# Optimization experiments

Measured on AMD Instinct MI355X. Metric: run time of the kernel, lower is better.

The kernel has to match this reference:

```python
import jax, jax.numpy as jnp
import numpy as np

EPS = 1e-6
FRAME_SEQLEN = 1560          # hardcoded in source kv-cache path
LOCAL_ATTN_SIZE = 4
MAX_ATTN = LOCAL_ATTN_SIZE * FRAME_SEQLEN  # 6240
NUM_HEADS = 12


def _ln(x, w=None, b=None):
    mu = jnp.mean(x, axis=-1, keepdims=True)
    var = jnp.mean(jnp.square(x - mu), axis=-1, keepdims=True)
    y = (x - mu) * jax.lax.rsqrt(var + EPS)
    return y * w + b if w is not None else y


def _rms(x, w):
    return x * jax.lax.rsqrt(jnp.mean(jnp.square(x), axis=-1, keepdims=True) + EPS) * w


def _rope_tables(freqs_real, freqs_imag, nf, hh, ww, start_frame, c):
    # split freqs columns into temporal / height / width parts, as in causal_rope_apply
    s0 = c - 2 * (c // 3)
    s1 = c // 3
    def build(tab):
        f0 = tab[start_frame:start_frame + nf, :s0]       # [nf, s0]
        f1 = tab[:hh, s0:s0 + s1]                          # [hh, s1]
        f2 = tab[:ww, s0 + s1:]                            # [ww, s1]
        return jnp.concatenate([
            jnp.broadcast_to(f0[:, None, None, :], (nf, hh, ww, s0)),
            jnp.broadcast_to(f1[None, :, None, :], (nf, hh, ww, s1)),
            jnp.broadcast_to(f2[None, None, :, :], (nf, hh, ww, s1)),
        ], axis=-1).reshape(nf * hh * ww, 1, c)
    return build(freqs_real), build(freqs_imag)


def _causal_rope(x, cos, sin):
    # x: [B, L, n, d] with interleaved (real, imag) pairs; cos/sin: [1, L, 1, c]
    B, L, n, d = x.shape
    c = d // 2
    xr = x.reshape(B, L, n, c, 2)
    a, b = xr[..., 0], xr[..., 1]
    out = jnp.stack([a * cos - b * sin, a * sin + b * cos], axis=-1)
    return out.reshape(B, L, n, d)


def _sdpa(q, k, v):
    scale = q.shape[-1] ** -0.5
    s = jnp.einsum('bqhd,bkhd->bhqk', q, k) * scale
    a = jax.nn.softmax(s, axis=-1)
    return jnp.einsum('bhqk,bkhd->bqhd', a, v)


def _forward(hidden_states, encoder_hidden_states, temb, freqs_real, freqs_imag,
             k_cache, v_cache, scale_shift_table,
             Wq, bq, Wk, bk, Wv, bv, Wo, bo, norm_q_w, norm_k_w,
             saln_w, saln_b,
             cWq, cbq, cWk, cbk, cWv, cbv, cWo, cbo, c_norm_q_w, c_norm_k_w,
             W1, b1, W2, b2,
             current_start, grid_h, grid_w):
    B, L, D = hidden_states.shape
    nf = temb.shape[1]
    fs = L // nf                     # == FRAME_SEQLEN
    H = NUM_HEADS
    hd = D // H
    c = hd // 2
    x = hidden_states.astype(jnp.float32)

    # AdaLN modulation per frame
    e = scale_shift_table + temb                     # [B, nf, 6, D]
    shift, scale, gate = e[:, :, 0:1], e[:, :, 1:2], e[:, :, 2:3]
    c_shift, c_scale, c_gate = e[:, :, 3:4], e[:, :, 4:5], e[:, :, 5:6]

    nh = (_ln(x).reshape(B, nf, fs, D) * (1 + scale) + shift).reshape(B, L, D)

    # self-attn projections + rms_norm_across_heads qk norm
    q = _rms(nh @ Wq.T + bq, norm_q_w).reshape(B, L, H, hd)
    k = _rms(nh @ Wk.T + bk, norm_k_w).reshape(B, L, H, hd)
    v = (nh @ Wv.T + bv).reshape(B, L, H, hd)

    # causal RoPE with temporal offset current_start // 1560
    start_frame = current_start // FRAME_SEQLEN
    cos, sin = _rope_tables(freqs_real, freqs_imag, nf, grid_h, grid_w, start_frame, c)
    cos, sin = cos[None], sin[None]                  # [1, L, 1, c]
    rq = _causal_rope(q, cos, sin)
    rk = _causal_rope(k, cos, sin)

    # kv-cache update (no-eviction branch: num_new + local_end_prev == cache size)
    kc = jax.lax.stop_gradient(k_cache).at[:, current_start:current_start + L].set(rk)
    vc = jax.lax.stop_gradient(v_cache).at[:, current_start:current_start + L].set(v)
    local_end = current_start + L
    win_lo = max(0, local_end - MAX_ATTN)
    attn = _sdpa(rq, kc[:, win_lo:local_end], vc[:, win_lo:local_end]).reshape(B, L, D)
    attn = attn @ Wo.T + bo

    # gated residual + affine LN (self_attn_residual_norm)
    x = x + (attn.reshape(B, nf, fs, D) * gate).reshape(B, L, D)
    n2 = _ln(x, saln_w, saln_b)

    # T2V cross attention
    ctx = encoder_hidden_states.astype(jnp.float32)
    Lc = ctx.shape[1]
    cq = _rms(n2 @ cWq.T + cbq, c_norm_q_w).reshape(B, L, H, hd)
    ck = _rms(ctx @ cWk.T + cbk, c_norm_k_w).reshape(B, Lc, H, hd)
    cv = (ctx @ cWv.T + cbv).reshape(B, Lc, H, hd)
    ca = _sdpa(cq, ck, cv).reshape(B, L, D) @ cWo.T + cbo

    # residual + LN with c_scale/c_shift modulation (cross_attn_residual_norm)
    x = x + ca
    n3 = (_ln(x).reshape(B, nf, fs, D) * (1 + c_scale) + c_shift).reshape(B, L, D)

    # FFN (gelu tanh) + gated residual (MulAdd)
    ff = jax.nn.gelu(n3 @ W1.T + b1, approximate=True) @ W2.T + b2
    x = x + (ff.reshape(B, nf, fs, D) * c_gate).reshape(B, L, D)
    return x


def setup_inputs() -> dict:
    key = jax.random.key(0)
    D, FF, H = 1536, 8960, NUM_HEADS
    NF, FS = 2, FRAME_SEQLEN
    L = NF * FS
    CACHE = MAX_ATTN
    CTX = 512
    hd = D // H
    c = hd // 2
    ks = iter(jax.random.split(key, 40))
    def nrm(shape, s=1.0):
        return jax.random.normal(next(ks), shape, jnp.float32) * s

    def part(dim):
        inv = 1.0 / (10000.0 ** (np.arange(0, dim, 2, dtype=np.float64) / dim))
        f = np.outer(np.arange(1024, dtype=np.float64), inv)
        return np.cos(f), np.sin(f)
    c0, s0 = part(2 * (c - 2 * (c // 3)))
    c1, s1 = part(2 * (c // 3))
    c2, s2 = part(2 * (c // 3))
    freqs_real = jnp.asarray(np.concatenate([c0, c1, c2], axis=1), jnp.float32)  # [1024, 64]
    freqs_imag = jnp.asarray(np.concatenate([s0, s1, s2], axis=1), jnp.float32)

    return dict(
        hidden_states=nrm((1, L, D)),
        encoder_hidden_states=nrm((1, CTX, D)),
        temb=nrm((1, NF, 6, D), 0.5),
        freqs_real=freqs_real, freqs_imag=freqs_imag,
        k_cache=nrm((1, CACHE, H, hd), 0.5),
        v_cache=nrm((1, CACHE, H, hd), 0.5),
        scale_shift_table=nrm((1, 6, D), D ** -0.5),
        Wq=nrm((D, D), 0.02), bq=jnp.zeros((D,), jnp.float32),
        Wk=nrm((D, D), 0.02), bk=jnp.zeros((D,), jnp.float32),
        Wv=nrm((D, D), 0.02), bv=jnp.zeros((D,), jnp.float32),
        Wo=nrm((D, D), 0.02), bo=jnp.zeros((D,), jnp.float32),
        norm_q_w=jnp.ones((D,), jnp.float32), norm_k_w=jnp.ones((D,), jnp.float32),
        saln_w=jnp.ones((D,), jnp.float32), saln_b=jnp.zeros((D,), jnp.float32),
        cWq=nrm((D, D), 0.02), cbq=jnp.zeros((D,), jnp.float32),
        cWk=nrm((D, D), 0.02), cbk=jnp.zeros((D,), jnp.float32),
        cWv=nrm((D, D), 0.02), cbv=jnp.zeros((D,), jnp.float32),
        cWo=nrm((D, D), 0.02), cbo=jnp.zeros((D,), jnp.float32),
        c_norm_q_w=jnp.ones((D,), jnp.float32), c_norm_k_w=jnp.ones((D,), jnp.float32),
        W1=nrm((FF, D), 0.02), b1=jnp.zeros((FF,), jnp.float32),
        W2=nrm((D, FF), 0.02), b2=jnp.zeros((D,), jnp.float32),
        current_start=2 * FS, grid_h=30, grid_w=52,
    )


def reference(hidden_states, encoder_hidden_states, temb, freqs_real, freqs_imag,
              k_cache, v_cache, scale_shift_table,
              Wq, bq, Wk, bk, Wv, bv, Wo, bo, norm_q_w, norm_k_w,
              saln_w, saln_b,
              cWq, cbq, cWk, cbk, cWv, cbv, cWo, cbo, c_norm_q_w, c_norm_k_w,
              W1, b1, W2, b2,
              current_start, grid_h, grid_w):
    return _forward(hidden_states, encoder_hidden_states, temb, freqs_real, freqs_imag,
                    k_cache, v_cache, scale_shift_table,
                    Wq, bq, Wk, bk, Wv, bv, Wo, bo, norm_q_w, norm_k_w,
                    saln_w, saln_b,
                    cWq, cbq, cWk, cbk, cWv, cbv, cWo, cbo, c_norm_q_w, c_norm_k_w,
                    W1, b1, W2, b2,
                    current_start, grid_h, grid_w)
```

## Files before the change

kernel.cpp:

```cpp
#include <hip/hip_runtime.h>
#include <hip/hip_bf16.h>
#include <stdint.h>

typedef uint16_t u16;
typedef uint32_t u32;
typedef float    f32x4  __attribute__((ext_vector_type(4)));
typedef __bf16   bf16x8 __attribute__((ext_vector_type(8)));
typedef u16      u16x8  __attribute__((ext_vector_type(8)));
typedef u16      u16x4  __attribute__((ext_vector_type(4)));
typedef float    f32x4v __attribute__((ext_vector_type(4)));

#define KSTR 6272
#define KHS  802816

__device__ __forceinline__ u16 f2bf(float f) {
    u32 u = __builtin_bit_cast(u32, f);
    u32 r = u + 0x7fffu + ((u >> 16) & 1u);
    return (u16)(r >> 16);
}
__device__ __forceinline__ float bfbits2f(u32 ubits) {
    return __builtin_bit_cast(float, ubits << 16);
}
__device__ __forceinline__ u32 cvtpk(float a, float b) {
    u32 r;
    asm("v_cvt_pk_bf16_f32 %0, %1, %2" : "=v"(r) : "v"(a), "v"(b));
    return r;
}
__device__ __forceinline__ bf16x8 loadb8(const u16* p) {
    u16x8 u = *(const u16x8*)p;
    return __builtin_bit_cast(bf16x8, u);
}
__device__ __forceinline__ f32x4 mfma16(bf16x8 a, bf16x8 b, f32x4 c) {
    return __builtin_amdgcn_mfma_f32_16x16x32_bf16(a, b, c, 0, 0, 0);
}
__device__ __forceinline__ void gload16(const u16* gp, u16* lp) {
    __builtin_amdgcn_global_load_lds((const __attribute__((address_space(1))) void*)gp,
                                     (__attribute__((address_space(3))) void*)lp, 16, 0, 0);
}
__device__ __forceinline__ float blockSum(float v, volatile float* buf, int t) {
#pragma unroll
    for (int o = 1; o < 64; o <<= 1) v += __shfl_xor(v, o);
    if ((t & 63) == 0) buf[t >> 6] = v;
    __syncthreads();
    float r = buf[0] + buf[1] + buf[2] + buf[3];
    __syncthreads();
    return r;
}

struct ConvJob { const float* s; u16* d; int n4; };
struct ConvJobs { ConvJob j[12]; int cnt; };

__global__ void k_conv(ConvJobs js) {
    int tid = blockIdx.x * blockDim.x + threadIdx.x;
    int stride = gridDim.x * blockDim.x;
    for (int q = 0; q < js.cnt; q++) {
        const f32x4v* s = (const f32x4v*)js.j[q].s;
        u16x4* d = (u16x4*)js.j[q].d;
        int n4 = js.j[q].n4;
        for (int i = tid; i < n4; i += stride) {
            f32x4v v = s[i];
            u16x4 o;
            o[0] = f2bf(v[0]); o[1] = f2bf(v[1]); o[2] = f2bf(v[2]); o[3] = f2bf(v[3]);
            d[i] = o;
        }
    }
}

__global__ void k_mod(const float* __restrict__ sst, const float* __restrict__ temb, float* __restrict__ e) {
    int i = blockIdx.x * 256 + threadIdx.x;
    if (i < 18432) e[i] = sst[i % 9216] + temb[i];
}

__global__ void k_cachecvt(const float* __restrict__ kc, const float* __restrict__ vc,
                           u16* __restrict__ Ka, u16* __restrict__ Va) {
    int b = blockIdx.x;
    int hd = (b % 6) * 256 + threadIdx.x;
    int p0 = (b / 6) * 4;
    int h = hd >> 7, d = hd & 127;
    u16x4 vv;
#pragma unroll
    for (int j = 0; j < 4; j++) {
        long src = (long)(p0 + j) * 1536 + hd;
        Ka[(long)h * KHS + (long)(p0 + j) * 128 + d] = f2bf(kc[src]);
        vv[j] = f2bf(vc[src]);
    }
    *(u16x4*)&Va[(long)h * KHS + (long)d * KSTR + p0] = vv;
}

__global__ void k_zpad(u16* __restrict__ Ka, u16* __restrict__ Va) {
    int i = blockIdx.x * 256 + threadIdx.x;
    int h = i >> 12, rem = i & 4095, row = rem >> 7, d = rem & 127;
    Ka[(long)h * KHS + (long)(6240 + row) * 128 + d] = 0;
    Va[(long)h * KHS + (long)d * KSTR + 6240 + row] = 0;
}

__global__ __launch_bounds__(256) void k_ln(const float* __restrict__ x, u16* __restrict__ out,
                                            const float* __restrict__ mulp, const float* __restrict__ addp,
                                            int perFrame, int plusOne) {
    __shared__ float buf[4];
    const int row = blockIdx.x, t = threadIdx.x;
    const float* xr = x + (long)row * 1536;
    float v[6];
    float s = 0.f;
#pragma unroll
    for (int k = 0; k < 6; k++) { v[k] = xr[t + k * 256]; s += v[k]; }
    s = blockSum(s, buf, t);
    float mu = s * (1.f / 1536.f);
    float q = 0.f;
#pragma unroll
    for (int k = 0; k < 6; k++) { float d = v[k] - mu; q += d * d; }
    q = blockSum(q, buf, t);
    float inv = rsqrtf(q * (1.f / 1536.f) + 1e-6f);
    const int fo = perFrame ? (row / 1560) * 9216 : 0;
    u16* orow = out + (long)row * 1536;
    float add1 = plusOne ? 1.f : 0.f;
#pragma unroll
    for (int k = 0; k < 6; k++) {
        int c = t + k * 256;
        float m = mulp[fo + c] + add1;
        float y = (v[k] - mu) * inv * m + addp[fo + c];
        orow[c] = f2bf(y);
    }
}

__global__ __launch_bounds__(256) void k_rmsrope(const u16* __restrict__ in, int ld, int colOff,
                                                 const float* __restrict__ bias,
                                                 const float* __restrict__ w,
                                                 u16* __restrict__ out, long headStride,
                                                 const float* __restrict__ fr, const float* __restrict__ fi,
                                                 int doRope) {
    __shared__ float buf[4];
    const int row = blockIdx.x, t = threadIdx.x;
    const u32* xr = (const u32*)(in + (long)row * ld + colOff);
    const float2* b2 = (const float2*)bias;
    float px[3], py[3];
    float ss = 0.f;
#pragma unroll
    for (int i = 0; i < 3; i++) {
        u32 u = xr[t * 3 + i];
        float2 bb = b2[t * 3 + i];
        px[i] = bfbits2f(u & 0xffffu) + bb.x;
        py[i] = bfbits2f(u >> 16) + bb.y;
        ss += px[i] * px[i] + py[i] * py[i];
    }
    ss = blockSum(ss, buf, t);
    float inv = rsqrtf(ss * (1.f / 1536.f) + 1e-6f);
    int frame = 0, gh = 0, gw = 0;
    if (doRope) { frame = row / 1560; int rem = row - frame * 1560; gh = rem / 52; gw = rem - gh * 52; }
    const float2* w2 = (const float2*)w;
#pragma unroll
    for (int i = 0; i < 3; i++) {
        int jg = t * 3 + i;
        int hh = jg >> 6, j = jg & 63;
        float2 ww = w2[jg];
        float a = px[i] * inv * ww.x, b = py[i] * inv * ww.y;
        float oa = a, ob = b;
        if (doRope) {
            int fidx = (j < 22) ? (2 + frame) : ((j < 43) ? gh : gw);
            float cs = fr[fidx * 64 + j], sn = fi[fidx * 64 + j];
            oa = a * cs - b * sn;
            ob = a * sn + b * cs;
        }
        u16* dst = out + (long)hh * headStride + (long)row * 128 + j * 2;
        dst[0] = f2bf(oa);
        dst[1] = f2bf(ob);
    }
}

__global__ void k_scatterT(const u16* __restrict__ in, int ld, int colOff,
                           const float* __restrict__ bias, u16* __restrict__ outT,
                           int vstride, int posOff) {
    int hd = blockIdx.x * 256 + threadIdx.x;
    int r0 = blockIdx.y * 4;
    int h = hd >> 7, d = hd & 127;
    float bi = bias[hd];
    u16x4 pk;
#pragma unroll
    for (int j = 0; j < 4; j++)
        pk[j] = f2bf(bfbits2f(in[(long)(r0 + j) * ld + colOff + hd]) + bi);
    *(u16x4*)&outT[(long)h * 128 * vstride + (long)d * vstride + posOff + r0] = pk;
}

struct GemmP {
    const u16* A; const u16* B; void* C;
    const float* bias; const float* gate; const float* resid;
    int M, N, K, ldA, ldB, ldC, kChunk;
};

template <int EPI, int BM>
__global__ __launch_bounds__(256) void k_gemm(GemmP g) {
    constexpr int WM = BM / 2;
    constexpr int TM = BM / 32;
    __shared__ alignas(16) u16 As[BM * 32];
    __shared__ alignas(16) u16 Bs[128 * 32];
    const int t = threadIdx.x;
    const int w = t >> 6, l = t & 63, lr = l & 15, lg = l >> 4;
    const int wm = w >> 1, wn = w & 1;
    const long m0 = (long)blockIdx.y * BM, n0 = (long)blockIdx.x * 128;
    f32x4 acc[TM][4];
#pragma unroll
    for (int a = 0; a < TM; a++)
#pragma unroll
        for (int b = 0; b < 4; b++) acc[a][b] = f32x4{0.f, 0.f, 0.f, 0.f};

    const int rowU = t >> 2, c8 = t & 3;
    long arow[2], brow[2];
#pragma unroll
    for (int i = 0; i < 2; i++) {
        long r = m0 + rowU + i * 64;
        if (r > (long)g.M - 1) r = g.M - 1;
        arow[i] = r;
        brow[i] = n0 + rowU + i * 64;
    }

    const int kBeg = blockIdx.z * g.kChunk;
    const int kEnd = min(g.K, kBeg + g.kChunk);
    for (int k0 = kBeg; k0 < kEnd; k0 += 32) {
        __syncthreads();
#pragma unroll
        for (int i = 0; i < BM / 64; i++)
            gload16(g.A + arow[i] * (long)g.ldA + k0 + c8 * 8, &As[(i * 256 + w * 64) * 8]);
#pragma unroll
        for (int i = 0; i < 2; i++)
            gload16(g.B + brow[i] * (long)g.ldB + k0 + c8 * 8, &Bs[(i * 256 + w * 64) * 8]);
        __syncthreads();
        bf16x8 am[TM], bn[4];
#pragma unroll
        for (int mi = 0; mi < TM; mi++) am[mi] = loadb8(&As[(wm * WM + mi * 16 + lr) * 32 + lg * 8]);
#pragma unroll
        for (int ni = 0; ni < 4; ni++) bn[ni] = loadb8(&Bs[(wn * 64 + ni * 16 + lr) * 32 + lg * 8]);
#pragma unroll
        for (int mi = 0; mi < TM; mi++)
#pragma unroll
            for (int ni = 0; ni < 4; ni++)
                acc[mi][ni] = mfma16(am[mi], bn[ni], acc[mi][ni]);
    }

#pragma unroll
    for (int mi = 0; mi < TM; mi++) {
#pragma unroll
        for (int ni = 0; ni < 4; ni++) {
            long col = n0 + wn * 64 + ni * 16 + lr;
            float bi = g.bias ? g.bias[col] : 0.f;
#pragma unroll
            for (int r = 0; r < 4; r++) {
                long row = m0 + wm * WM + mi * 16 + lg * 4 + r;
                if (row >= g.M) continue;
                float v = acc[mi][ni][r] + bi;
                if constexpr (EPI == 0) {
                    ((float*)g.C)[row * g.ldC + col] = v;
                } else if constexpr (EPI == 1) {
                    ((u16*)g.C)[row * g.ldC + col] = f2bf(v);
                } else if constexpr (EPI == 2) {
                    float x3 = v * v * v;
                    float gl = 0.5f * v * (1.f + tanhf(0.79788456080286536f * (v + 0.044715f * x3)));
                    ((u16*)g.C)[row * g.ldC + col] = f2bf(gl);
                } else if constexpr (EPI == 3) {
                    float gt = g.gate ? g.gate[(row / 1560) * 9216 + col] : 1.f;
                    ((float*)g.C)[row * g.ldC + col] = g.resid[row * g.ldC + col] + v * gt;
                } else {
                    ((float*)g.C)[(long)blockIdx.z * ((long)g.M * g.ldC) + row * g.ldC + col] = v;
                }
            }
        }
    }
}

__global__ void k_gcomb(const float* __restrict__ P, int S, long MN4,
                        const float* __restrict__ bias, const float* __restrict__ gate,
                        const float* __restrict__ resid, float* __restrict__ out) {
    long i = (long)blockIdx.x * 256 + threadIdx.x;
    if (i >= MN4) return;
    f32x4v a = ((const f32x4v*)P)[i];
#pragma unroll 3
    for (int s = 1; s < S; s++) {
        f32x4v b = ((const f32x4v*)P)[(long)s * MN4 + i];
        a[0] += b[0]; a[1] += b[1]; a[2] += b[2]; a[3] += b[3];
    }
    long e0 = i * 4;
    int col = (int)(e0 % 1536);
    int fo = (int)((e0 / 1536) / 1560) * 9216;
    f32x4v r = ((const f32x4v*)resid)[i];
#pragma unroll
    for (int j = 0; j < 4; j++)
        r[j] += (a[j] + bias[col + j]) * gate[fo + col + j];
    ((f32x4v*)out)[i] = r;
}

__global__ void k_sumbf(const float* __restrict__ P, int S, long N4, u16* __restrict__ out) {
    long i = (long)blockIdx.x * 256 + threadIdx.x;
    if (i >= N4) return;
    f32x4v a = ((const f32x4v*)P)[i];
#pragma unroll 3
    for (int s = 1; s < S; s++) {
        f32x4v b = ((const f32x4v*)P)[(long)s * N4 + i];
        a[0] += b[0]; a[1] += b[1]; a[2] += b[2]; a[3] += b[3];
    }
    u16x4 o;
    o[0] = f2bf(a[0]); o[1] = f2bf(a[1]); o[2] = f2bf(a[2]); o[3] = f2bf(a[3]);
    ((u16x4*)out)[i] = o;
}

__global__ __launch_bounds__(256) void k_flash(const u16* __restrict__ Qb, const u16* __restrict__ Kb,
                                               const u16* __restrict__ Vtg,
                                               u16* __restrict__ Opart, float2* __restrict__ ms,
                                               int kvStride, int kvLen, int qlen,
                                               int splitIters, int totIters) {
    __shared__ alignas(16) u16 Kt[64 * 136];
    __shared__ alignas(16) u16 Vt[128 * 72];
    __shared__ alignas(16) u16 Pt[4][32 * 40];
    const int t = threadIdx.x;
    const int w = t >> 6, l = t & 63, lr = l & 15, lg = l >> 4;
    const int head = blockIdx.y, z = blockIdx.z;
    const long q0 = (long)blockIdx.x * 128;
    const u16* Qh = Qb + (long)head * qlen * 128;
    const u16* Kh = Kb + (long)head * (long)kvStride * 128;
    const u16* Vh = Vtg + (long)head * (long)kvStride * 128;
    constexpr float SCL2 = 0.08838834764831845f * 1.44269504088896f;

    bf16x8 aq[2][4];
#pragma unroll
    for (int wq = 0; wq < 2; wq++)
#pragma unroll
        for (int c = 0; c < 4; c++) {
            long row = q0 + w * 32 + wq * 16 + lr;
            if (row > (long)qlen - 1) row = qlen - 1;
            aq[wq][c] = loadb8(Qh + row * 128 + c * 32 + lg * 8);
        }

    f32x4 o[2][8];
    float mrow[2] = {-1e30f, -1e30f}, srow[2] = {0.f, 0.f};
#pragma unroll
    for (int wq = 0; wq < 2; wq++)
#pragma unroll
        for (int db = 0; db < 8; db++) o[wq][db] = f32x4{0.f, 0.f, 0.f, 0.f};

    const int krow = t >> 2, kcol = (t & 3) * 32;
    const int vrow = t >> 1, vcol = (t & 1) * 32;
    u16x8 pkr[4], pvr[4];

    const int it0 = z * splitIters;
    const int itN = min(totIters, it0 + splitIters);

    auto loadTile = [&](int kt) {
        long k0 = (long)kt * 64;
        const u16* kp = Kh + (k0 + krow) * 128 + kcol;
#pragma unroll
        for (int j = 0; j < 4; j++) pkr[j] = *(const u16x8*)(kp + j * 8);
        const u16* vp = Vh + (long)vrow * kvStride + k0 + vcol;
#pragma unroll
        for (int j = 0; j < 4; j++) pvr[j] = *(const u16x8*)(vp + j * 8);
    };
    auto writeTile = [&]() {
#pragma unroll
        for (int j = 0; j < 4; j++) *(u16x8*)&Kt[krow * 136 + kcol + j * 8] = pkr[j];
#pragma unroll
        for (int j = 0; j < 4; j++) *(u16x8*)&Vt[vrow * 72 + vcol + j * 8] = pvr[j];
    };

    loadTile(it0);
    writeTile();
    __syncthreads();

    for (int kt = it0; kt < itN; kt++) {
        const bool hasNext = (kt + 1 < itN);
        if (hasNext) loadTile(kt + 1);
        const int lim = kvLen - kt * 64;

#pragma unroll
        for (int h2 = 0; h2 < 2; h2++) {
            f32x4 s[2][2];
            __builtin_amdgcn_s_setprio(1);
#pragma unroll
            for (int kh = 0; kh < 2; kh++) {
                bf16x8 kf[4];
#pragma unroll
                for (int cb = 0; cb < 4; cb++)
                    kf[cb] = loadb8(&Kt[(h2 * 32 + kh * 16 + lr) * 136 + cb * 32 + lg * 8]);
#pragma unroll
                for (int wq = 0; wq < 2; wq++) {
                    f32x4 acc = f32x4{0.f, 0.f, 0.f, 0.f};
#pragma unroll
                    for (int cb = 0; cb < 4; cb++) acc = mfma16(kf[cb], aq[wq][cb], acc);
                    s[wq][kh] = acc;
                }
            }
            __builtin_amdgcn_s_setprio(0);

            const int sublim = lim - h2 * 32;
#pragma unroll
            for (int wq = 0; wq < 2; wq++) {
                float pm = fmaxf(fmaxf(fmaxf(s[wq][0][0], s[wq][0][1]), fmaxf(s[wq][0][2], s[wq][0][3])),
                                 fmaxf(fmaxf(s[wq][1][0], s[wq][1][1]), fmaxf(s[wq][1][2], s[wq][1][3])));
                pm = fmaxf(pm, __shfl_xor(pm, 16));
                pm = fmaxf(pm, __shfl_xor(pm, 32));
                float pm2 = pm * SCL2;
                if (__any(pm2 > mrow[wq] + 8.f)) {
                    float nm = fmaxf(mrow[wq], pm2);
                    float fsc = exp2f(mrow[wq] - nm);
                    mrow[wq] = nm;
                    srow[wq] *= fsc;
#pragma unroll
                    for (int db = 0; db < 8; db++) {
                        f32x4 t4 = o[wq][db];
                        t4[0] *= fsc; t4[1] *= fsc; t4[2] *= fsc; t4[3] *= fsc;
                        o[wq][db] = t4;
                    }
                }
                float p[8];
#pragma unroll
                for (int kh = 0; kh < 2; kh++)
#pragma unroll
                    for (int r = 0; r < 4; r++)
                        p[kh * 4 + r] = exp2f(fmaf(s[wq][kh][r], SCL2, -mrow[wq]));
                if (sublim < 32) {
#pragma unroll
                    for (int kh = 0; kh < 2; kh++)
#pragma unroll
                        for (int r = 0; r < 4; r++)
                            if (kh * 16 + lg * 4 + r >= sublim) p[kh * 4 + r] = 0.f;
                }
                float ts = ((p[0] + p[1]) + (p[2] + p[3])) + ((p[4] + p[5]) + (p[6] + p[7]));
                ts += __shfl_xor(ts, 16);
                ts += __shfl_xor(ts, 32);
                srow[wq] += ts;
                u32 w0 = cvtpk(p[0], p[1]), w1 = cvtpk(p[2], p[3]);
                u32 w2 = cvtpk(p[4], p[5]), w3 = cvtpk(p[6], p[7]);
                u16* pp = &Pt[w][(wq * 16 + lr) * 40 + lg * 4];
                *(u32*)pp = w0;
                *(u32*)(pp + 2) = w1;
                *(u32*)(pp + 16) = w2;
                *(u32*)(pp + 18) = w3;
            }

            bf16x8 pb0 = loadb8(&Pt[w][lr * 40 + lg * 8]);
            bf16x8 pb1 = loadb8(&Pt[w][(16 + lr) * 40 + lg * 8]);
            __builtin_amdgcn_s_setprio(1);
#pragma unroll
            for (int db = 0; db < 8; db++) {
                bf16x8 vf = loadb8(&Vt[(db * 16 + lr) * 72 + h2 * 32 + lg * 8]);
                o[0][db] = mfma16(vf, pb0, o[0][db]);
                o[1][db] = mfma16(vf, pb1, o[1][db]);
            }
            __builtin_amdgcn_s_setprio(0);
        }
        __syncthreads();
        if (hasNext) writeTile();
        __syncthreads();
    }

    const long part = ((long)z * 12 + head) * qlen;
#pragma unroll
    for (int wq = 0; wq < 2; wq++) {
        long row = q0 + w * 32 + wq * 16 + lr;
        if (row < qlen) {
            if (lg == 0) {
                float2 v; v.x = mrow[wq]; v.y = srow[wq];
                ms[part + row] = v;
            }
#pragma unroll
            for (int db = 0; db < 8; db++) {
                u16x4 pk;
#pragma unroll
                for (int r = 0; r < 4; r++) pk[r] = f2bf(o[wq][db][r]);
                *(u16x4*)&Opart[(part + row) * 128 + db * 16 + lg * 4] = pk;
            }
        }
    }
}

__global__ __launch_bounds__(256) void k_combine(const u16* __restrict__ Opart, const float2* __restrict__ ms,
                                                 u16* __restrict__ Ob, int qlen, int S) {
    int idx = blockIdx.x * 4 + (threadIdx.x >> 6);
    int l = threadIdx.x & 63;
    int h = idx / qlen, q = idx - h * qlen;
    float2 mm[6];
    float M = -1e30f;
    for (int s = 0; s < S; s++) {
        mm[s] = ms[((long)s * 12 + h) * qlen + q];
        M = fmaxf(M, mm[s].x);
    }
    float den = 0.f, a0 = 0.f, a1 = 0.f;
    for (int s = 0; s < S; s++) {
        float wgt = exp2f(mm[s].x - M);
        den += wgt * mm[s].y;
        u32 two = *(const u32*)&Opart[(((long)s * 12 + h) * qlen + q) * 128 + l * 2];
        a0 += wgt * bfbits2f(two & 0xffffu);
        a1 += wgt * bfbits2f(two >> 16);
    }
    float inv = 1.f / den;
    u32 o = ((u32)f2bf(a1 * inv) << 16) | (u32)f2bf(a0 * inv);
    *(u32*)&Ob[(long)q * 1536 + h * 128 + l * 2] = o;
}

extern "C" void kernel_launch(void* const* d_in, const int* in_sizes, int n_in,
                              void* d_out, int out_size, void* d_ws, size_t ws_size,
                              hipStream_t stream) {
    const float* hs    = (const float*)d_in[0];
    const float* ctx   = (const float*)d_in[1];
    const float* temb  = (const float*)d_in[2];
    const float* fr    = (const float*)d_in[3];
    const float* fi    = (const float*)d_in[4];
    const float* kcache= (const float*)d_in[5];
    const float* vcache= (const float*)d_in[6];
    const float* sst   = (const float*)d_in[7];
    const float* Wq = (const float*)d_in[8],  *bq = (const float*)d_in[9];
    const float* Wk = (const float*)d_in[10], *bk = (const float*)d_in[11];
    const float* Wv = (const float*)d_in[12], *bv = (const float*)d_in[13];
    const float* Wo = (const float*)d_in[14], *bo = (const float*)d_in[15];
    const float* nqw = (const float*)d_in[16], *nkw = (const float*)d_in[17];
    const float* salnw = (const float*)d_in[18], *salnb = (const float*)d_in[19];
    const float* cWq = (const float*)d_in[20], *cbq = (const float*)d_in[21];
    const float* cWk = (const float*)d_in[22], *cbk = (const float*)d_in[23];
    const float* cWv = (const float*)d_in[24], *cbv = (const float*)d_in[25];
    const float* cWo = (const float*)d_in[26], *cbo = (const float*)d_in[27];
    const float* cnqw = (const float*)d_in[28], *cnkw = (const float*)d_in[29];
    const float* W1 = (const float*)d_in[30], *b1 = (const float*)d_in[31];
    const float* W2 = (const float*)d_in[32], *b2 = (const float*)d_in[33];
    float* out = (float*)d_out;

    char* base = (char*)d_ws;
    size_t off = 0;
    auto alloc = [&](size_t bytes) -> char* {
        char* p = base + off;
        off = (off + bytes + 255) & ~(size_t)255;
        return p;
    };
    float* e   = (float*)alloc(18432 * 4);
    u16* nbuf  = (u16*)alloc((size_t)3120 * 1536 * 2);
    u16* lin   = (u16*)alloc((size_t)3120 * 4608 * 2);
    u16* Qb    = (u16*)alloc((size_t)12 * 3120 * 128 * 2);
    u16* Ka    = (u16*)alloc((size_t)12 * KSTR * 128 * 2);
    u16* Va    = (u16*)alloc((size_t)12 * KSTR * 128 * 2);
    u16* attnb = (u16*)alloc((size_t)3120 * 1536 * 2);
    float* X1  = (float*)alloc((size_t)3120 * 1536 * 4);
    u16* CKb   = (u16*)alloc((size_t)12 * 512 * 128 * 2);
    u16* CVt   = (u16*)alloc((size_t)12 * 512 * 128 * 2);
    u16* H1    = (u16*)alloc((size_t)3120 * 8960 * 2);
    u16* wqkv_b= (u16*)alloc((size_t)4608 * 1536 * 2);
    u16* wo_b  = (u16*)alloc((size_t)1536 * 1536 * 2);
    u16* cwq_b = (u16*)alloc((size_t)1536 * 1536 * 2);
    u16* cwkv_b= (u16*)alloc((size_t)3072 * 1536 * 2);
    u16* cwo_b = (u16*)alloc((size_t)1536 * 1536 * 2);
    u16* w1_b  = (u16*)alloc((size_t)8960 * 1536 * 2);
    u16* w2_b  = (u16*)alloc((size_t)8960 * 1536 * 2);
    u16* ctxb  = (u16*)alloc((size_t)512 * 1536 * 2);

    u16* Opart = H1;
    float2* msb = (float2*)lin;
    float* pbuf = (float*)lin;
    float* cpart = (float*)H1;

    ConvJobs cj{};
    auto setj = [&](int i, const float* s, u16* d, int n) { cj.j[i].s = s; cj.j[i].d = d; cj.j[i].n4 = n / 4; };
    setj(0, Wq, wqkv_b, 1536 * 1536);
    setj(1, Wk, wqkv_b + (size_t)1536 * 1536, 1536 * 1536);
    setj(2, Wv, wqkv_b + (size_t)2 * 1536 * 1536, 1536 * 1536);
    setj(3, Wo, wo_b, 1536 * 1536);
    setj(4, cWq, cwq_b, 1536 * 1536);
    setj(5, cWk, cwkv_b, 1536 * 1536);
    setj(6, cWv, cwkv_b + (size_t)1536 * 1536, 1536 * 1536);
    setj(7, cWo, cwo_b, 1536 * 1536);
    setj(8, W1, w1_b, 8960 * 1536);
    setj(9, W2, w2_b, 8960 * 1536);
    setj(10, ctx, ctxb, 512 * 1536);
    cj.cnt = 11;
    k_conv<<<2048, 256, 0, stream>>>(cj);

    k_mod<<<72, 256, 0, stream>>>(sst, temb, e);
    k_cachecvt<<<4680, 256, 0, stream>>>(kcache, vcache, Ka, Va);
    k_zpad<<<192, 256, 0, stream>>>(Ka, Va);

    k_ln<<<3120, 256, 0, stream>>>(hs, nbuf, e + 1536, e + 0, 1, 1);

    GemmP gqkv{nbuf, wqkv_b, lin, nullptr, nullptr, nullptr, 3120, 4608, 1536, 1536, 1536, 4608, 1536};
    k_gemm<1, 128><<<dim3(36, 25), 256, 0, stream>>>(gqkv);
    k_rmsrope<<<3120, 256, 0, stream>>>(lin, 4608, 0, bq, nqw, Qb, (long)3120 * 128, fr, fi, 1);
    k_rmsrope<<<3120, 256, 0, stream>>>(lin, 4608, 1536, bk, nkw, Ka + (size_t)3120 * 128, (long)KHS, fr, fi, 1);
    k_scatterT<<<dim3(6, 780), 256, 0, stream>>>(lin, 4608, 3072, bv, Va, KSTR, 3120);

    k_flash<<<dim3(25, 12, 5), 256, 0, stream>>>(Qb, Ka, Va, Opart, msb, KSTR, 6240, 3120, 20, 98);
    k_combine<<<9360, 256, 0, stream>>>(Opart, msb, attnb, 3120, 5);

    GemmP gwo{attnb, wo_b, X1, bo, e + 2 * 1536, hs, 3120, 1536, 1536, 1536, 1536, 1536, 1536};
    k_gemm<3, 64><<<dim3(12, 49), 256, 0, stream>>>(gwo);

    k_ln<<<3120, 256, 0, stream>>>(X1, nbuf, salnw, salnb, 0, 0);

    GemmP gcq{nbuf, cwq_b, lin, nullptr, nullptr, nullptr, 3120, 1536, 1536, 1536, 1536, 1536, 1536};
    k_gemm<1, 64><<<dim3(12, 49), 256, 0, stream>>>(gcq);
    k_rmsrope<<<3120, 256, 0, stream>>>(lin, 1536, 0, cbq, cnqw, Qb, (long)3120 * 128, fr, fi, 0);

    GemmP gckv{ctxb, cwkv_b, cpart, nullptr, nullptr, nullptr, 512, 3072, 1536, 1536, 1536, 3072, 384};
    k_gemm<5, 64><<<dim3(24, 8, 4), 256, 0, stream>>>(gckv);
    k_sumbf<<<1536, 256, 0, stream>>>(cpart, 4, 393216, lin);
    k_rmsrope<<<512, 256, 0, stream>>>(lin, 3072, 0, cbk, cnkw, CKb, (long)512 * 128, fr, fi, 0);
    k_scatterT<<<dim3(6, 128), 256, 0, stream>>>(lin, 3072, 1536, cbv, CVt, 512, 0);

    k_flash<<<dim3(25, 12, 4), 256, 0, stream>>>(Qb, CKb, CVt, Opart, msb, 512, 512, 3120, 2, 8);
    k_combine<<<9360, 256, 0, stream>>>(Opart, msb, attnb, 3120, 4);

    GemmP gcwo{attnb, cwo_b, X1, cbo, nullptr, X1, 3120, 1536, 1536, 1536, 1536, 1536, 1536};
    k_gemm<3, 64><<<dim3(12, 49), 256, 0, stream>>>(gcwo);

    k_ln<<<3120, 256, 0, stream>>>(X1, nbuf, e + 4 * 1536, e + 3 * 1536, 1, 1);

    GemmP g1{nbuf, w1_b, H1, b1, nullptr, nullptr, 3120, 8960, 1536, 1536, 1536, 8960, 1536};
    k_gemm<2, 128><<<dim3(70, 25), 256, 0, stream>>>(g1);

    GemmP g2{H1, w2_b, pbuf, nullptr, nullptr, nullptr, 3120, 1536, 8960, 8960, 8960, 1536, 2240};
    k_gemm<5, 128><<<dim3(12, 25, 4), 256, 0, stream>>>(g2);
    k_gcomb<<<4680, 256, 0, stream>>>(pbuf, 4, 1198080, b2, e + 5 * 1536, X1, out);
}
```

Measured before the change: 1.278 ms.

## Read K/V fragments directly from global memory in flash attention, drop LDS staging and padding

The flash kernel no longer stages 64-row K and V tiles through shared memory with double-buffered register prefetch and two barriers per iteration. Each wave now loads its K and V MFMA fragments straight from global memory in 32-key steps. Because 6240 is a multiple of 32, the KV buffers are no longer padded to 6272, so the zero-pad kernel and the tail masking are removed. This cuts LDS traffic and block-wide syncs, but every wave in a block re-reads the same K/V from global/L2, and the V-transposed loads are strided by the row length.

```diff
diff --git a/kernel.cpp b/kernel.cpp
--- a/kernel.cpp
+++ b/kernel.cpp
@@ -10,8 +10,6 @@
 typedef u16      u16x4  __attribute__((ext_vector_type(4)));
 typedef float    f32x4v __attribute__((ext_vector_type(4)));
 
-#define KSTR 6272
-#define KHS  802816
 
 __device__ __forceinline__ u16 f2bf(float f) {
     u32 u = __builtin_bit_cast(u32, f);
@@ -81,17 +79,10 @@
 #pragma unroll
     for (int j = 0; j < 4; j++) {
         long src = (long)(p0 + j) * 1536 + hd;
-        Ka[(long)h * KHS + (long)(p0 + j) * 128 + d] = f2bf(kc[src]);
+        Ka[(long)h * 798720 + (long)(p0 + j) * 128 + d] = f2bf(kc[src]);
         vv[j] = f2bf(vc[src]);
     }
-    *(u16x4*)&Va[(long)h * KHS + (long)d * KSTR + p0] = vv;
-}
-
-__global__ void k_zpad(u16* __restrict__ Ka, u16* __restrict__ Va) {
-    int i = blockIdx.x * 256 + threadIdx.x;
-    int h = i >> 12, rem = i & 4095, row = rem >> 7, d = rem & 127;
-    Ka[(long)h * KHS + (long)(6240 + row) * 128 + d] = 0;
-    Va[(long)h * KHS + (long)d * KSTR + 6240 + row] = 0;
+    *(u16x4*)&Va[(long)h * 798720 + (long)d * 6240 + p0] = vv;
 }
 
 __global__ __launch_bounds__(256) void k_ln(const float* __restrict__ x, u16* __restrict__ out,
@@ -304,10 +295,7 @@
 __global__ __launch_bounds__(256) void k_flash(const u16* __restrict__ Qb, const u16* __restrict__ Kb,
                                                const u16* __restrict__ Vtg,
                                                u16* __restrict__ Opart, float2* __restrict__ ms,
-                                               int kvStride, int kvLen, int qlen,
-                                               int splitIters, int totIters) {
-    __shared__ alignas(16) u16 Kt[64 * 136];
-    __shared__ alignas(16) u16 Vt[128 * 72];
+                                               int kvStride, int qlen, int splitIters, int totIters) {
     __shared__ alignas(16) u16 Pt[4][32 * 40];
     const int t = threadIdx.x;
     const int w = t >> 6, l = t & 63, lr = l & 15, lg = l >> 4;
@@ -335,118 +323,84 @@
 #pragma unroll
         for (int db = 0; db < 8; db++) o[wq][db] = f32x4{0.f, 0.f, 0.f, 0.f};
 
-    const int krow = t >> 2, kcol = (t & 3) * 32;
-    const int vrow = t >> 1, vcol = (t & 1) * 32;
-    u16x8 pkr[4], pvr[4];
-
     const int it0 = z * splitIters;
     const int itN = min(totIters, it0 + splitIters);
-
-    auto loadTile = [&](int kt) {
-        long k0 = (long)kt * 64;
-        const u16* kp = Kh + (k0 + krow) * 128 + kcol;
-#pragma unroll
-        for (int j = 0; j < 4; j++) pkr[j] = *(const u16x8*)(kp + j * 8);
-        const u16* vp = Vh + (long)vrow * kvStride + k0 + vcol;
-#pragma unroll
-        for (int j = 0; j < 4; j++) pvr[j] = *(const u16x8*)(vp + j * 8);
-    };
-    auto writeTile = [&]() {
-#pragma unroll
-        for (int j = 0; j < 4; j++) *(u16x8*)&Kt[krow * 136 + kcol + j * 8] = pkr[j];
-#pragma unroll
-        for (int j = 0; j < 4; j++) *(u16x8*)&Vt[vrow * 72 + vcol + j * 8] = pvr[j];
-    };
-
-    loadTile(it0);
-    writeTile();
-    __syncthreads();
-
     for (int kt = it0; kt < itN; kt++) {
-        const bool hasNext = (kt + 1 < itN);
-        if (hasNext) loadTile(kt + 1);
-        const int lim = kvLen - kt * 64;
-
-#pragma unroll
-        for (int h2 = 0; h2 < 2; h2++) {
-            f32x4 s[2][2];
+        const long k0 = (long)kt * 32;
+
+        f32x4 s[2][2];
+        {
+            bf16x8 kf[2][4];
+#pragma unroll
+            for (int kh = 0; kh < 2; kh++)
+#pragma unroll
+                for (int cb = 0; cb < 4; cb++)
+                    kf[kh][cb] = loadb8(Kh + (k0 + kh * 16 + lr) * 128 + cb * 32 + lg * 8);
             __builtin_amdgcn_s_setprio(1);
 #pragma unroll
-            for (int kh = 0; kh < 2; kh++) {
-                bf16x8 kf[4];
-#pragma unroll
-                for (int cb = 0; cb < 4; cb++)
-                    kf[cb] = loadb8(&Kt[(h2 * 32 + kh * 16 + lr) * 136 + cb * 32 + lg * 8]);
+            for (int kh = 0; kh < 2; kh++)
 #pragma unroll
                 for (int wq = 0; wq < 2; wq++) {
                     f32x4 acc = f32x4{0.f, 0.f, 0.f, 0.f};
 #pragma unroll
-                    for (int cb = 0; cb < 4; cb++) acc = mfma16(kf[cb], aq[wq][cb], acc);
+                    for (int cb = 0; cb < 4; cb++) acc = mfma16(kf[kh][cb], aq[wq][cb], acc);
                     s[wq][kh] = acc;
                 }
+            __builtin_amdgcn_s_setprio(0);
+        }
+
+        bf16x8 vf[8];
+#pragma unroll
+        for (int db = 0; db < 8; db++)
+            vf[db] = loadb8(Vh + (long)(db * 16 + lr) * kvStride + k0 + lg * 8);
+
+#pragma unroll
+        for (int wq = 0; wq < 2; wq++) {
+            float pm = fmaxf(fmaxf(fmaxf(s[wq][0][0], s[wq][0][1]), fmaxf(s[wq][0][2], s[wq][0][3])),
+                             fmaxf(fmaxf(s[wq][1][0], s[wq][1][1]), fmaxf(s[wq][1][2], s[wq][1][3])));
+            pm = fmaxf(pm, __shfl_xor(pm, 16));
+            pm = fmaxf(pm, __shfl_xor(pm, 32));
+            float pm2 = pm * SCL2;
+            if (__any(pm2 > mrow[wq] + 8.f)) {
+                float nm = fmaxf(mrow[wq], pm2);
+                float fsc = exp2f(mrow[wq] - nm);
+                mrow[wq] = nm;
+                srow[wq] *= fsc;
+#pragma unroll
+                for (int db = 0; db < 8; db++) {
+                    f32x4 t4 = o[wq][db];
+                    t4[0] *= fsc; t4[1] *= fsc; t4[2] *= fsc; t4[3] *= fsc;
+                    o[wq][db] = t4;
+                }
             }
-            __builtin_amdgcn_s_setprio(0);
-
-            const int sublim = lim - h2 * 32;
-#pragma unroll
-            for (int wq = 0; wq < 2; wq++) {
-                float pm = fmaxf(fmaxf(fmaxf(s[wq][0][0], s[wq][0][1]), fmaxf(s[wq][0][2], s[wq][0][3])),
-                                 fmaxf(fmaxf(s[wq][1][0], s[wq][1][1]), fmaxf(s[wq][1][2], s[wq][1][3])));
-                pm = fmaxf(pm, __shfl_xor(pm, 16));
-                pm = fmaxf(pm, __shfl_xor(pm, 32));
-                float pm2 = pm * SCL2;
-                if (__any(pm2 > mrow[wq] + 8.f)) {
-                    float nm = fmaxf(mrow[wq], pm2);
-                    float fsc = exp2f(mrow[wq] - nm);
-                    mrow[wq] = nm;
-                    srow[wq] *= fsc;
-#pragma unroll
-                    for (int db = 0; db < 8; db++) {
-                        f32x4 t4 = o[wq][db];
-                        t4[0] *= fsc; t4[1] *= fsc; t4[2] *= fsc; t4[3] *= fsc;
-                        o[wq][db] = t4;
-                    }
-                }
-                float p[8];
-#pragma unroll
-                for (int kh = 0; kh < 2; kh++)
-#pragma unroll
-                    for (int r = 0; r < 4; r++)
-                        p[kh * 4 + r] = exp2f(fmaf(s[wq][kh][r], SCL2, -mrow[wq]));
-                if (sublim < 32) {
-#pragma unroll
-                    for (int kh = 0; kh < 2; kh++)
-#pragma unroll
-                        for (int r = 0; r < 4; r++)
-                            if (kh * 16 + lg * 4 + r >= sublim) p[kh * 4 + r] = 0.f;
-                }
-                float ts = ((p[0] + p[1]) + (p[2] + p[3])) + ((p[4] + p[5]) + (p[6] + p[7]));
-                ts += __shfl_xor(ts, 16);
-                ts += __shfl_xor(ts, 32);
-                srow[wq] += ts;
-                u32 w0 = cvtpk(p[0], p[1]), w1 = cvtpk(p[2], p[3]);
-                u32 w2 = cvtpk(p[4], p[5]), w3 = cvtpk(p[6], p[7]);
-                u16* pp = &Pt[w][(wq * 16 + lr) * 40 + lg * 4];
-                *(u32*)pp = w0;
-                *(u32*)(pp + 2) = w1;
-                *(u32*)(pp + 16) = w2;
-                *(u32*)(pp + 18) = w3;
-            }
-
-            bf16x8 pb0 = loadb8(&Pt[w][lr * 40 + lg * 8]);
-            bf16x8 pb1 = loadb8(&Pt[w][(16 + lr) * 40 + lg * 8]);
-            __builtin_amdgcn_s_setprio(1);
-#pragma unroll
-            for (int db = 0; db < 8; db++) {
-                bf16x8 vf = loadb8(&Vt[(db * 16 + lr) * 72 + h2 * 32 + lg * 8]);
-                o[0][db] = mfma16(vf, pb0, o[0][db]);
-                o[1][db] = mfma16(vf, pb1, o[1][db]);
-            }
-            __builtin_amdgcn_s_setprio(0);
-        }
-        __syncthreads();
-        if (hasNext) writeTile();
-        __syncthreads();
+            float p[8];
+#pragma unroll
+            for (int kh = 0; kh < 2; kh++)
+#pragma unroll
+                for (int r = 0; r < 4; r++)
+                    p[kh * 4 + r] = exp2f(fmaf(s[wq][kh][r], SCL2, -mrow[wq]));
+            float ts = ((p[0] + p[1]) + (p[2] + p[3])) + ((p[4] + p[5]) + (p[6] + p[7]));
+            ts += __shfl_xor(ts, 16);
+            ts += __shfl_xor(ts, 32);
+            srow[wq] += ts;
+            u32 w0 = cvtpk(p[0], p[1]), w1 = cvtpk(p[2], p[3]);
+            u32 w2 = cvtpk(p[4], p[5]), w3 = cvtpk(p[6], p[7]);
+            u16* pp = &Pt[w][(wq * 16 + lr) * 40 + lg * 4];
+            *(u32*)pp = w0;
+            *(u32*)(pp + 2) = w1;
+            *(u32*)(pp + 16) = w2;
+            *(u32*)(pp + 18) = w3;
+        }
+
+        bf16x8 pb0 = loadb8(&Pt[w][lr * 40 + lg * 8]);
+        bf16x8 pb1 = loadb8(&Pt[w][(16 + lr) * 40 + lg * 8]);
+        __builtin_amdgcn_s_setprio(1);
+#pragma unroll
+        for (int db = 0; db < 8; db++) {
+            o[0][db] = mfma16(vf[db], pb0, o[0][db]);
+            o[1][db] = mfma16(vf[db], pb1, o[1][db]);
+        }
+        __builtin_amdgcn_s_setprio(0);
     }
 
     const long part = ((long)z * 12 + head) * qlen;
@@ -530,8 +484,8 @@
     u16* nbuf  = (u16*)alloc((size_t)3120 * 1536 * 2);
     u16* lin   = (u16*)alloc((size_t)3120 * 4608 * 2);
     u16* Qb    = (u16*)alloc((size_t)12 * 3120 * 128 * 2);
-    u16* Ka    = (u16*)alloc((size_t)12 * KSTR * 128 * 2);
-    u16* Va    = (u16*)alloc((size_t)12 * KSTR * 128 * 2);
+    u16* Ka    = (u16*)alloc((size_t)12 * 6240 * 128 * 2);
+    u16* Va    = (u16*)alloc((size_t)12 * 6240 * 128 * 2);
     u16* attnb = (u16*)alloc((size_t)3120 * 1536 * 2);
     float* X1  = (float*)alloc((size_t)3120 * 1536 * 4);
     u16* CKb   = (u16*)alloc((size_t)12 * 512 * 128 * 2);
@@ -569,17 +523,16 @@
 
     k_mod<<<72, 256, 0, stream>>>(sst, temb, e);
     k_cachecvt<<<4680, 256, 0, stream>>>(kcache, vcache, Ka, Va);
-    k_zpad<<<192, 256, 0, stream>>>(Ka, Va);
 
     k_ln<<<3120, 256, 0, stream>>>(hs, nbuf, e + 1536, e + 0, 1, 1);
 
     GemmP gqkv{nbuf, wqkv_b, lin, nullptr, nullptr, nullptr, 3120, 4608, 1536, 1536, 1536, 4608, 1536};
     k_gemm<1, 128><<<dim3(36, 25), 256, 0, stream>>>(gqkv);
     k_rmsrope<<<3120, 256, 0, stream>>>(lin, 4608, 0, bq, nqw, Qb, (long)3120 * 128, fr, fi, 1);
-    k_rmsrope<<<3120, 256, 0, stream>>>(lin, 4608, 1536, bk, nkw, Ka + (size_t)3120 * 128, (long)KHS, fr, fi, 1);
-    k_scatterT<<<dim3(6, 780), 256, 0, stream>>>(lin, 4608, 3072, bv, Va, KSTR, 3120);
-
-    k_flash<<<dim3(25, 12, 5), 256, 0, stream>>>(Qb, Ka, Va, Opart, msb, KSTR, 6240, 3120, 20, 98);
+    k_rmsrope<<<3120, 256, 0, stream>>>(lin, 4608, 1536, bk, nkw, Ka + (size_t)3120 * 128, (long)6240 * 128, fr, fi, 1);
+    k_scatterT<<<dim3(6, 780), 256, 0, stream>>>(lin, 4608, 3072, bv, Va, 6240, 3120);
+
+    k_flash<<<dim3(25, 12, 5), 256, 0, stream>>>(Qb, Ka, Va, Opart, msb, 6240, 3120, 39, 195);
     k_combine<<<9360, 256, 0, stream>>>(Opart, msb, attnb, 3120, 5);
 
     GemmP gwo{attnb, wo_b, X1, bo, e + 2 * 1536, hs, 3120, 1536, 1536, 1536, 1536, 1536, 1536};
@@ -597,7 +550,7 @@
     k_rmsrope<<<512, 256, 0, stream>>>(lin, 3072, 0, cbk, cnkw, CKb, (long)512 * 128, fr, fi, 0);
     k_scatterT<<<dim3(6, 128), 256, 0, stream>>>(lin, 3072, 1536, cbv, CVt, 512, 0);
 
-    k_flash<<<dim3(25, 12, 4), 256, 0, stream>>>(Qb, CKb, CVt, Opart, msb, 512, 512, 3120, 2, 8);
+    k_flash<<<dim3(25, 12, 4), 256, 0, stream>>>(Qb, CKb, CVt, Opart, msb, 512, 3120, 4, 16);
     k_combine<<<9360, 256, 0, stream>>>(Opart, msb, attnb, 3120, 4);
 
     GemmP gcwo{attnb, cwo_b, X1, cbo, nullptr, X1, 3120, 1536, 1536, 1536, 1536, 1536, 1536};
```

Result: faster. 1.212 ms (-5.1%).
